# Kernel tuning notes

Hardware: AMD Instinct MI355X
Metric: run time of the kernel (lower is better)

Reference implementation:

```python
import jax, jax.numpy as jnp
from jax import lax
import numpy as np

BS, L, D, K, R, VOCAB = 4096, 200, 64, 4, 3, 100000
DROP = jnp.float32(-(1 << 31))


def squash(caps):
    # caps: (bs, K, D)
    n = jnp.linalg.norm(caps, axis=2, keepdims=True)   # (bs, K, 1)
    n2 = n * n
    return n2 / ((1.0 + n2) * n + 1e-9) * caps


def setup_inputs() -> dict:
    key = jax.random.key(0)
    ks = jax.random.split(key, 8)
    his = jax.random.randint(ks[0], (BS, L), 0, VOCAB)                     # item ids, 0 = pad
    E = jax.random.normal(ks[1], (VOCAB, D), dtype=jnp.float32)            # itemEmbeds.weight
    S = jax.random.normal(ks[2], (D, D), dtype=jnp.float32)                # bilinear map S
    B0 = jax.random.normal(ks[3], (K, L), dtype=jnp.float32)               # routing logits
    lim1 = 1.0 / np.sqrt(D)
    W1 = jax.random.uniform(ks[4], (D, 4 * D), jnp.float32, -lim1, lim1)   # dense1 (in, out)
    b1 = jax.random.uniform(ks[5], (4 * D,), jnp.float32, -lim1, lim1)
    lim2 = 1.0 / np.sqrt(4 * D)
    W2 = jax.random.uniform(ks[6], (4 * D, D), jnp.float32, -lim2, lim2)   # dense2 (in, out)
    b2 = jax.random.uniform(ks[7], (D,), jnp.float32, -lim2, lim2)
    return {"his": his, "E": E, "S": S, "B0": B0, "W1": W1, "b1": b1, "W2": W2, "b2": b2}


def reference(his, E, S, B0, W1, b1, W2, b2):
    bs = his.shape[0]
    # padding_idx=0 -> embedding row 0 is zero
    E = E.at[0].set(0.0)
    mask = (his != 0)[:, None, :]                       # (bs, 1, L), broadcasts over K
    hisP = jnp.einsum('bld,de->ble', E[his], S)         # (bs, L, D)
    hisPd = lax.stop_gradient(hisP)                     # routing updates run under no_grad
    B = jnp.broadcast_to(lax.stop_gradient(B0)[None], (bs, K, L))
    for _ in range(R - 1):
        W = jax.nn.softmax(jnp.where(mask, B, DROP), axis=2)   # (bs, K, L)
        caps = squash(jnp.einsum('bkl,bld->bkd', W, hisPd))
        B = B + jnp.einsum('bkd,bld->bkl', caps, hisPd)
    W = jax.nn.softmax(jnp.where(mask, B, DROP), axis=2)
    caps = squash(jnp.einsum('bkl,bld->bkd', W, hisP))         # differentiable last iter
    h = jax.nn.relu(jnp.einsum('bkd,df->bkf', caps, W1) + b1)
    return jnp.einsum('bkf,fd->bkd', h, W2) + b2               # (bs, K, D)
```

## Files before the change

### kernel.cpp

```cpp
#include <hip/hip_runtime.h>

#define LSEQ 200
#define KCAP 4
#define NVOC 100000

__device__ __forceinline__ void fma4(float4& a, float s, const float4& v) {
    a.x = fmaf(s, v.x, a.x); a.y = fmaf(s, v.y, a.y);
    a.z = fmaf(s, v.z, a.z); a.w = fmaf(s, v.w, a.w);
}

__global__ __launch_bounds__(256) void precompute_P(
    const float* __restrict__ E, const float* __restrict__ S,
    float* __restrict__ P)
{
    __shared__ __align__(16) float4 Sl4[1024];
    const int tid = threadIdx.x;
    #pragma unroll
    for (int t = tid; t < 1024; t += 256) Sl4[t] = ((const float4*)S)[t];
    __syncthreads();

    const int v = blockIdx.x * 256 + tid;
    const bool ok = (v < NVOC);
    const float4* __restrict__ Er = (const float4*)E + (size_t)(ok ? v : 0) * 16;

    float4 acc[16];
    #pragma unroll
    for (int j = 0; j < 16; j++) acc[j] = make_float4(0.f, 0.f, 0.f, 0.f);

    #pragma unroll 1
    for (int ec = 0; ec < 16; ec += 2) {
        float4 ea = Er[ec], eb = Er[ec + 1];
        float ev[8] = {ea.x, ea.y, ea.z, ea.w, eb.x, eb.y, eb.z, eb.w};
        #pragma unroll
        for (int e = 0; e < 8; e++) {
            const float4* Srow = Sl4 + (ec * 4 + e) * 16;
            #pragma unroll
            for (int j = 0; j < 16; j++) fma4(acc[j], ev[e], Srow[j]);
        }
    }
    if (ok) {
        float4* Pr = (float4*)P + (size_t)v * 16;
        if (v == 0) {
            #pragma unroll
            for (int j = 0; j < 16; j++) acc[j] = make_float4(0.f, 0.f, 0.f, 0.f);
        }
        #pragma unroll
        for (int j = 0; j < 16; j++) Pr[j] = acc[j];
    }
}

__global__ __launch_bounds__(256, 2) void mind_row(
    const int*   __restrict__ his, const float* __restrict__ P,
    const float* __restrict__ B0,  const float* __restrict__ W1,
    const float* __restrict__ b1,  const float* __restrict__ W2,
    const float* __restrict__ b2,  float* __restrict__ out)
{
    __shared__ __align__(16) float4 hisP4[LSEQ * 17];
    __shared__ __align__(16) float  W4[LSEQ * 4];
    __shared__ __align__(16) float  Bm[KCAP * LSEQ];
    __shared__ __align__(16) float  caps4[64 * 4];
    __shared__ __align__(16) float4 capsT4[KCAP * 16];
    __shared__ __align__(16) float4 part4[16 * 17];
    __shared__ float bigneg[LSEQ];
    __shared__ int   idxs[LSEQ];

    const int b = blockIdx.x, tid = threadIdx.x;
    const int lane = tid & 63, wv = tid >> 6;
    const int q = lane >> 4, r = lane & 15;

    for (int l = tid; l < LSEQ; l += 256) {
        int id = his[b * LSEQ + l];
        idxs[l]   = id;
        bigneg[l] = (id != 0) ? 0.f : -1e30f;
    }
    for (int t = tid; t < KCAP * LSEQ; t += 256) Bm[t] = B0[t];
    __syncthreads();

    float4 hp4[13];
    const float4* P4 = (const float4*)P;
    #pragma unroll
    for (int i = 0; i < 13; i++) {
        int  l     = wv * 50 + i * 4 + q;
        bool valid = (i < 12) || (q < 2);
        int  lc    = valid ? l : 0;
        float4 vv  = P4[(size_t)idxs[lc] * 16 + r];
        if (!valid) vv = make_float4(0.f, 0.f, 0.f, 0.f);
        hp4[i] = vv;
        if (valid) hisP4[l * 17 + r] = vv;
    }
    __syncthreads();

    for (int rr = 0; rr < 3; rr++) {
        {
            const float* Bk = Bm + wv * LSEQ;
            float x0 = Bk[lane]       + bigneg[lane];
            float x1 = Bk[lane + 64]  + bigneg[lane + 64];
            float x2 = Bk[lane + 128] + bigneg[lane + 128];
            float x3 = (lane < 8) ? (Bk[lane + 192] + bigneg[lane + 192]) : -3.0e38f;
            float m = fmaxf(fmaxf(x0, x1), fmaxf(x2, x3));
            #pragma unroll
            for (int off = 32; off; off >>= 1) m = fmaxf(m, __shfl_xor(m, off, 64));
            float e0 = __expf(x0 - m), e1 = __expf(x1 - m), e2 = __expf(x2 - m);
            float e3 = (lane < 8) ? __expf(x3 - m) : 0.f;
            float s = e0 + e1 + e2 + e3;
            #pragma unroll
            for (int off = 32; off; off >>= 1) s += __shfl_xor(s, off, 64);
            float inv = 1.f / s;
            W4[lane * 4 + wv]         = e0 * inv;
            W4[(lane + 64) * 4 + wv]  = e1 * inv;
            W4[(lane + 128) * 4 + wv] = e2 * inv;
            if (lane < 8) W4[(lane + 192) * 4 + wv] = e3 * inv;
        }
        __syncthreads();

        {
            float4 a0 = make_float4(0,0,0,0), a1 = a0, a2 = a0, a3 = a0;
            #pragma unroll
            for (int i = 0; i < 13; i++) {
                int l  = wv * 50 + i * 4 + q;
                int lc = (l < LSEQ - 1) ? l : (LSEQ - 1);
                float4 w = *(const float4*)(W4 + lc * 4);
                fma4(a0, w.x, hp4[i]); fma4(a1, w.y, hp4[i]);
                fma4(a2, w.z, hp4[i]); fma4(a3, w.w, hp4[i]);
            }
            #pragma unroll
            for (int off = 16; off <= 32; off <<= 1) {
                a0.x += __shfl_xor(a0.x, off, 64); a0.y += __shfl_xor(a0.y, off, 64);
                a0.z += __shfl_xor(a0.z, off, 64); a0.w += __shfl_xor(a0.w, off, 64);
                a1.x += __shfl_xor(a1.x, off, 64); a1.y += __shfl_xor(a1.y, off, 64);
                a1.z += __shfl_xor(a1.z, off, 64); a1.w += __shfl_xor(a1.w, off, 64);
                a2.x += __shfl_xor(a2.x, off, 64); a2.y += __shfl_xor(a2.y, off, 64);
                a2.z += __shfl_xor(a2.z, off, 64); a2.w += __shfl_xor(a2.w, off, 64);
                a3.x += __shfl_xor(a3.x, off, 64); a3.y += __shfl_xor(a3.y, off, 64);
                a3.z += __shfl_xor(a3.z, off, 64); a3.w += __shfl_xor(a3.w, off, 64);
            }
            if (q == 0) {
                part4[(wv * 4 + 0) * 17 + r] = a0;
                part4[(wv * 4 + 1) * 17 + r] = a1;
                part4[(wv * 4 + 2) * 17 + r] = a2;
                part4[(wv * 4 + 3) * 17 + r] = a3;
            }
        }
        __syncthreads();

        {
            const float* pf = (const float*)part4;
            float c = pf[(0 * 4 + wv) * 68 + lane] + pf[(1 * 4 + wv) * 68 + lane]
                    + pf[(2 * 4 + wv) * 68 + lane] + pf[(3 * 4 + wv) * 68 + lane];
            float n2 = c * c;
            #pragma unroll
            for (int off = 32; off; off >>= 1) n2 += __shfl_xor(n2, off, 64);
            float n  = sqrtf(n2);
            float sc = n2 / ((1.f + n2) * n + 1e-9f);
            c *= sc;
            caps4[lane * 4 + wv]          = c;
            ((float*)capsT4)[wv * 64 + lane] = c;
        }
        __syncthreads();

        if (rr < 2) {
            if (tid < LSEQ) {
                const int l = tid;
                float s0 = 0, s1 = 0, s2 = 0, s3 = 0;
                #pragma unroll
                for (int j = 0; j < 16; j++) {
                    float4 h  = hisP4[l * 17 + j];
                    float4 c0 = capsT4[j],      c1 = capsT4[16 + j];
                    float4 c2 = capsT4[32 + j], c3 = capsT4[48 + j];
                    s0 = fmaf(h.x, c0.x, fmaf(h.y, c0.y, fmaf(h.z, c0.z, fmaf(h.w, c0.w, s0))));
                    s1 = fmaf(h.x, c1.x, fmaf(h.y, c1.y, fmaf(h.z, c1.z, fmaf(h.w, c1.w, s1))));
                    s2 = fmaf(h.x, c2.x, fmaf(h.y, c2.y, fmaf(h.z, c2.z, fmaf(h.w, c2.w, s2))));
                    s3 = fmaf(h.x, c3.x, fmaf(h.y, c3.y, fmaf(h.z, c3.z, fmaf(h.w, c3.w, s3))));
                }
                Bm[l]       += s0;
                Bm[200 + l] += s1;
                Bm[400 + l] += s2;
                Bm[600 + l] += s3;
            }
            __syncthreads();
        }
    }

    float4* h44 = (float4*)hisP4;
    {
        const int f = tid;
        float h0 = 0, h1 = 0, h2 = 0, h3 = 0;
        #pragma unroll 8
        for (int d = 0; d < 64; d++) {
            float  w = W1[d * 256 + f];
            float4 c = *(const float4*)(caps4 + d * 4);
            h0 = fmaf(c.x, w, h0); h1 = fmaf(c.y, w, h1);
            h2 = fmaf(c.z, w, h2); h3 = fmaf(c.w, w, h3);
        }
        float bb = b1[f];
        h44[f] = make_float4(fmaxf(h0 + bb, 0.f), fmaxf(h1 + bb, 0.f),
                             fmaxf(h2 + bb, 0.f), fmaxf(h3 + bb, 0.f));
    }
    __syncthreads();
    float* partf = (float*)part4;
    {
        float o0 = 0, o1 = 0, o2 = 0, o3 = 0;
        #pragma unroll 8
        for (int i = 0; i < 64; i++) {
            int f = wv * 64 + i;
            float  w  = W2[f * 64 + lane];
            float4 hv = h44[f];
            o0 = fmaf(hv.x, w, o0); o1 = fmaf(hv.y, w, o1);
            o2 = fmaf(hv.z, w, o2); o3 = fmaf(hv.w, w, o3);
        }
        partf[wv * 256 + lane]       = o0;
        partf[wv * 256 + 64 + lane]  = o1;
        partf[wv * 256 + 128 + lane] = o2;
        partf[wv * 256 + 192 + lane] = o3;
    }
    __syncthreads();
    {
        float o = partf[wv * 64 + lane]       + partf[256 + wv * 64 + lane]
                + partf[512 + wv * 64 + lane] + partf[768 + wv * 64 + lane];
        out[b * 256 + tid] = o + b2[lane];
    }
}

extern "C" void kernel_launch(void* const* d_in, const int* in_sizes, int n_in,
                              void* d_out, int out_size, void* d_ws, size_t ws_size,
                              hipStream_t stream) {
    const int*   his = (const int*)  d_in[0];
    const float* E   = (const float*)d_in[1];
    const float* S   = (const float*)d_in[2];
    const float* B0  = (const float*)d_in[3];
    const float* W1  = (const float*)d_in[4];
    const float* b1  = (const float*)d_in[5];
    const float* W2  = (const float*)d_in[6];
    const float* b2  = (const float*)d_in[7];
    float* out = (float*)d_out;
    float* P   = (float*)d_ws;

    precompute_P<<<(NVOC + 255) / 256, 256, 0, stream>>>(E, S, P);
    mind_row<<<4096, 256, 0, stream>>>(his, P, B0, W1, b1, W2, b2, out);
}
```

Baseline: 256.3 us.

## Drop hisP LDS copy, reuse register-held rows with shuffles; split P precompute across waves

The routing-logit update now takes history rows from the registers loaded during the gather and reduces the dot products with xor shuffles, so the large padded hisP shared-memory buffer and one barrier are gone. With less LDS per block, launch bounds rise to 4 blocks per CU to increase occupancy. The embedding projection kernel now gives each wave 16 of the 64 output columns, reading S straight from global/cache instead of LDS. This lowers registers per thread in that kernel. The cost is more shuffle traffic and four times as many E row reads in the precompute.

```diff
diff --git a/kernel.cpp b/kernel.cpp
--- a/kernel.cpp
+++ b/kernel.cpp
@@ -13,54 +13,56 @@
     const float* __restrict__ E, const float* __restrict__ S,
     float* __restrict__ P)
 {
-    __shared__ __align__(16) float4 Sl4[1024];
-    const int tid = threadIdx.x;
+    const int tid  = threadIdx.x;
+    const int lane = tid & 63;
+    const int wvu  = __builtin_amdgcn_readfirstlane(tid >> 6);
+    const int row  = blockIdx.x * 64 + lane;
+    const bool ok  = (row < NVOC);
+
+    const float4* __restrict__ Er = (const float4*)E + (size_t)(ok ? row : 0) * 16;
+    const float4* __restrict__ S4 = (const float4*)S + wvu * 4;
+
+    float4 acc[4];
     #pragma unroll
-    for (int t = tid; t < 1024; t += 256) Sl4[t] = ((const float4*)S)[t];
-    __syncthreads();
-
-    const int v = blockIdx.x * 256 + tid;
-    const bool ok = (v < NVOC);
-    const float4* __restrict__ Er = (const float4*)E + (size_t)(ok ? v : 0) * 16;
-
-    float4 acc[16];
-    #pragma unroll
-    for (int j = 0; j < 16; j++) acc[j] = make_float4(0.f, 0.f, 0.f, 0.f);
-
-    #pragma unroll 1
-    for (int ec = 0; ec < 16; ec += 2) {
-        float4 ea = Er[ec], eb = Er[ec + 1];
-        float ev[8] = {ea.x, ea.y, ea.z, ea.w, eb.x, eb.y, eb.z, eb.w};
+    for (int j = 0; j < 4; j++) acc[j] = make_float4(0.f, 0.f, 0.f, 0.f);
+
+    #pragma unroll 4
+    for (int ec = 0; ec < 16; ec++) {
+        float4 ev = Er[ec];
+        float e4[4] = {ev.x, ev.y, ev.z, ev.w};
         #pragma unroll
-        for (int e = 0; e < 8; e++) {
-            const float4* Srow = Sl4 + (ec * 4 + e) * 16;
-            #pragma unroll
-            for (int j = 0; j < 16; j++) fma4(acc[j], ev[e], Srow[j]);
+        for (int u = 0; u < 4; u++) {
+            const int e = ec * 4 + u;
+            float4 s0 = S4[e * 16 + 0];
+            float4 s1 = S4[e * 16 + 1];
+            float4 s2 = S4[e * 16 + 2];
+            float4 s3 = S4[e * 16 + 3];
+            fma4(acc[0], e4[u], s0); fma4(acc[1], e4[u], s1);
+            fma4(acc[2], e4[u], s2); fma4(acc[3], e4[u], s3);
         }
     }
     if (ok) {
-        float4* Pr = (float4*)P + (size_t)v * 16;
-        if (v == 0) {
-            #pragma unroll
-            for (int j = 0; j < 16; j++) acc[j] = make_float4(0.f, 0.f, 0.f, 0.f);
-        }
-        #pragma unroll
-        for (int j = 0; j < 16; j++) Pr[j] = acc[j];
-    }
-}
-
-__global__ __launch_bounds__(256, 2) void mind_row(
+        if (row == 0) {
+            #pragma unroll
+            for (int j = 0; j < 4; j++) acc[j] = make_float4(0.f, 0.f, 0.f, 0.f);
+        }
+        float4* Pr = (float4*)P + (size_t)row * 16 + wvu * 4;
+        Pr[0] = acc[0]; Pr[1] = acc[1]; Pr[2] = acc[2]; Pr[3] = acc[3];
+    }
+}
+
+__global__ __launch_bounds__(256, 4) void mind_row(
     const int*   __restrict__ his, const float* __restrict__ P,
     const float* __restrict__ B0,  const float* __restrict__ W1,
     const float* __restrict__ b1,  const float* __restrict__ W2,
     const float* __restrict__ b2,  float* __restrict__ out)
 {
-    __shared__ __align__(16) float4 hisP4[LSEQ * 17];
     __shared__ __align__(16) float  W4[LSEQ * 4];
     __shared__ __align__(16) float  Bm[KCAP * LSEQ];
     __shared__ __align__(16) float  caps4[64 * 4];
     __shared__ __align__(16) float4 capsT4[KCAP * 16];
     __shared__ __align__(16) float4 part4[16 * 17];
+    __shared__ __align__(16) float4 h44[256];
     __shared__ float bigneg[LSEQ];
     __shared__ int   idxs[LSEQ];
 
@@ -86,9 +88,7 @@
         float4 vv  = P4[(size_t)idxs[lc] * 16 + r];
         if (!valid) vv = make_float4(0.f, 0.f, 0.f, 0.f);
         hp4[i] = vv;
-        if (valid) hisP4[l * 17 + r] = vv;
-    }
-    __syncthreads();
+    }
 
     for (int rr = 0; rr < 3; rr++) {
         {
@@ -153,35 +153,40 @@
             float n  = sqrtf(n2);
             float sc = n2 / ((1.f + n2) * n + 1e-9f);
             c *= sc;
-            caps4[lane * 4 + wv]          = c;
+            caps4[lane * 4 + wv]             = c;
             ((float*)capsT4)[wv * 64 + lane] = c;
         }
         __syncthreads();
 
         if (rr < 2) {
-            if (tid < LSEQ) {
-                const int l = tid;
-                float s0 = 0, s1 = 0, s2 = 0, s3 = 0;
+            float4 c0 = capsT4[0 * 16 + r];
+            float4 c1 = capsT4[1 * 16 + r];
+            float4 c2 = capsT4[2 * 16 + r];
+            float4 c3 = capsT4[3 * 16 + r];
+            #pragma unroll
+            for (int i = 0; i < 13; i++) {
+                float4 v = hp4[i];
+                float p0 = fmaf(v.x, c0.x, fmaf(v.y, c0.y, fmaf(v.z, c0.z, v.w * c0.w)));
+                float p1 = fmaf(v.x, c1.x, fmaf(v.y, c1.y, fmaf(v.z, c1.z, v.w * c1.w)));
+                float p2 = fmaf(v.x, c2.x, fmaf(v.y, c2.y, fmaf(v.z, c2.z, v.w * c2.w)));
+                float p3 = fmaf(v.x, c3.x, fmaf(v.y, c3.y, fmaf(v.z, c3.z, v.w * c3.w)));
                 #pragma unroll
-                for (int j = 0; j < 16; j++) {
-                    float4 h  = hisP4[l * 17 + j];
-                    float4 c0 = capsT4[j],      c1 = capsT4[16 + j];
-                    float4 c2 = capsT4[32 + j], c3 = capsT4[48 + j];
-                    s0 = fmaf(h.x, c0.x, fmaf(h.y, c0.y, fmaf(h.z, c0.z, fmaf(h.w, c0.w, s0))));
-                    s1 = fmaf(h.x, c1.x, fmaf(h.y, c1.y, fmaf(h.z, c1.z, fmaf(h.w, c1.w, s1))));
-                    s2 = fmaf(h.x, c2.x, fmaf(h.y, c2.y, fmaf(h.z, c2.z, fmaf(h.w, c2.w, s2))));
-                    s3 = fmaf(h.x, c3.x, fmaf(h.y, c3.y, fmaf(h.z, c3.z, fmaf(h.w, c3.w, s3))));
+                for (int off = 1; off < 16; off <<= 1) {
+                    p0 += __shfl_xor(p0, off, 64);
+                    p1 += __shfl_xor(p1, off, 64);
+                    p2 += __shfl_xor(p2, off, 64);
+                    p3 += __shfl_xor(p3, off, 64);
                 }
-                Bm[l]       += s0;
-                Bm[200 + l] += s1;
-                Bm[400 + l] += s2;
-                Bm[600 + l] += s3;
+                if (r < 4 && ((i < 12) || (q < 2))) {
+                    int l = wv * 50 + i * 4 + q;
+                    float p = (r == 0) ? p0 : (r == 1) ? p1 : (r == 2) ? p2 : p3;
+                    Bm[r * 200 + l] += p;
+                }
             }
             __syncthreads();
         }
     }
 
-    float4* h44 = (float4*)hisP4;
     {
         const int f = tid;
         float h0 = 0, h1 = 0, h2 = 0, h3 = 0;
@@ -235,6 +240,6 @@
     float* out = (float*)d_out;
     float* P   = (float*)d_ws;
 
-    precompute_P<<<(NVOC + 255) / 256, 256, 0, stream>>>(E, S, P);
+    precompute_P<<<(NVOC + 63) / 64, 256, 0, stream>>>(E, S, P);
     mind_row<<<4096, 256, 0, stream>>>(his, P, B0, W1, b1, W2, b2, out);
 }
```

After: 262.2 us. +2.3%, slower.

## Fuse projection into routing kernel by applying S to capsules, not embeddings

Applied to the files above, without the earlier changes.

Drops the precompute pass that multiplied all 100k vocabulary embeddings by S. The single fused kernel gathers raw embedding rows and moves S onto the capsule side: it forms W·E, then multiplies by S, and for the routing update it uses E·(S·caps). Routing logits and masks also move from shared memory into registers. This removes a 25.6 MB write and read of the projected table plus the vocab-wide GEMM, at the cost of small per-row 64x64 matvecs against S read from global memory in every routing iteration.

```diff
diff --git a/kernel.cpp b/kernel.cpp
--- a/kernel.cpp
+++ b/kernel.cpp
@@ -2,110 +2,72 @@
 
 #define LSEQ 200
 #define KCAP 4
-#define NVOC 100000
 
 __device__ __forceinline__ void fma4(float4& a, float s, const float4& v) {
     a.x = fmaf(s, v.x, a.x); a.y = fmaf(s, v.y, a.y);
     a.z = fmaf(s, v.z, a.z); a.w = fmaf(s, v.w, a.w);
 }
 
-__global__ __launch_bounds__(256) void precompute_P(
-    const float* __restrict__ E, const float* __restrict__ S,
-    float* __restrict__ P)
+__global__ __launch_bounds__(256, 2) void mind_fused(
+    const int*   __restrict__ his, const float* __restrict__ E,
+    const float* __restrict__ S,   const float* __restrict__ B0,
+    const float* __restrict__ W1,  const float* __restrict__ b1,
+    const float* __restrict__ W2,  const float* __restrict__ b2,
+    float* __restrict__ out)
 {
-    __shared__ __align__(16) float4 Sl4[1024];
-    const int tid = threadIdx.x;
-    #pragma unroll
-    for (int t = tid; t < 1024; t += 256) Sl4[t] = ((const float4*)S)[t];
-    __syncthreads();
-
-    const int v = blockIdx.x * 256 + tid;
-    const bool ok = (v < NVOC);
-    const float4* __restrict__ Er = (const float4*)E + (size_t)(ok ? v : 0) * 16;
-
-    float4 acc[16];
-    #pragma unroll
-    for (int j = 0; j < 16; j++) acc[j] = make_float4(0.f, 0.f, 0.f, 0.f);
-
-    #pragma unroll 1
-    for (int ec = 0; ec < 16; ec += 2) {
-        float4 ea = Er[ec], eb = Er[ec + 1];
-        float ev[8] = {ea.x, ea.y, ea.z, ea.w, eb.x, eb.y, eb.z, eb.w};
-        #pragma unroll
-        for (int e = 0; e < 8; e++) {
-            const float4* Srow = Sl4 + (ec * 4 + e) * 16;
-            #pragma unroll
-            for (int j = 0; j < 16; j++) fma4(acc[j], ev[e], Srow[j]);
-        }
-    }
-    if (ok) {
-        float4* Pr = (float4*)P + (size_t)v * 16;
-        if (v == 0) {
-            #pragma unroll
-            for (int j = 0; j < 16; j++) acc[j] = make_float4(0.f, 0.f, 0.f, 0.f);
-        }
-        #pragma unroll
-        for (int j = 0; j < 16; j++) Pr[j] = acc[j];
-    }
-}
-
-__global__ __launch_bounds__(256, 2) void mind_row(
-    const int*   __restrict__ his, const float* __restrict__ P,
-    const float* __restrict__ B0,  const float* __restrict__ W1,
-    const float* __restrict__ b1,  const float* __restrict__ W2,
-    const float* __restrict__ b2,  float* __restrict__ out)
-{
-    __shared__ __align__(16) float4 hisP4[LSEQ * 17];
+    __shared__ __align__(16) float4 Er4[LSEQ * 17];
     __shared__ __align__(16) float  W4[LSEQ * 4];
-    __shared__ __align__(16) float  Bm[KCAP * LSEQ];
+    __shared__ __align__(16) float4 part4[16 * 16];
+    __shared__ __align__(16) float  cbuf[256];
+    __shared__ __align__(16) float  capsL[256];
     __shared__ __align__(16) float  caps4[64 * 4];
-    __shared__ __align__(16) float4 capsT4[KCAP * 16];
-    __shared__ __align__(16) float4 part4[16 * 17];
-    __shared__ float bigneg[LSEQ];
-    __shared__ int   idxs[LSEQ];
+
+    int* idxs = (int*)cbuf;
 
     const int b = blockIdx.x, tid = threadIdx.x;
     const int lane = tid & 63, wv = tid >> 6;
     const int q = lane >> 4, r = lane & 15;
 
-    for (int l = tid; l < LSEQ; l += 256) {
-        int id = his[b * LSEQ + l];
-        idxs[l]   = id;
-        bigneg[l] = (id != 0) ? 0.f : -1e30f;
-    }
-    for (int t = tid; t < KCAP * LSEQ; t += 256) Bm[t] = B0[t];
-    __syncthreads();
+    for (int l = tid; l < LSEQ; l += 256) idxs[l] = his[b * LSEQ + l];
+    __syncthreads();
+
+    float Breg[4], msk[4];
+    #pragma unroll
+    for (int s = 0; s < 4; s++) {
+        int l = lane + 64 * s;
+        bool in = (l < LSEQ);
+        Breg[s] = in ? B0[wv * LSEQ + l] : 0.f;
+        msk[s]  = (in && idxs[l] != 0) ? 0.f : -3.0e38f;
+    }
 
     float4 hp4[13];
-    const float4* P4 = (const float4*)P;
+    const float4* E4 = (const float4*)E;
     #pragma unroll
     for (int i = 0; i < 13; i++) {
         int  l     = wv * 50 + i * 4 + q;
         bool valid = (i < 12) || (q < 2);
-        int  lc    = valid ? l : 0;
-        float4 vv  = P4[(size_t)idxs[lc] * 16 + r];
-        if (!valid) vv = make_float4(0.f, 0.f, 0.f, 0.f);
+        int  lc    = valid ? l : (wv * 50);
+        int  id    = idxs[lc];
+        float4 vv  = E4[(size_t)id * 16 + r];
+        if (id == 0 || !valid) vv = make_float4(0.f, 0.f, 0.f, 0.f);
         hp4[i] = vv;
-        if (valid) hisP4[l * 17 + r] = vv;
+        if (valid) Er4[l * 17 + r] = vv;
     }
     __syncthreads();
 
     for (int rr = 0; rr < 3; rr++) {
         {
-            const float* Bk = Bm + wv * LSEQ;
-            float x0 = Bk[lane]       + bigneg[lane];
-            float x1 = Bk[lane + 64]  + bigneg[lane + 64];
-            float x2 = Bk[lane + 128] + bigneg[lane + 128];
-            float x3 = (lane < 8) ? (Bk[lane + 192] + bigneg[lane + 192]) : -3.0e38f;
+            float x0 = Breg[0] + msk[0], x1 = Breg[1] + msk[1];
+            float x2 = Breg[2] + msk[2], x3 = Breg[3] + msk[3];
             float m = fmaxf(fmaxf(x0, x1), fmaxf(x2, x3));
             #pragma unroll
             for (int off = 32; off; off >>= 1) m = fmaxf(m, __shfl_xor(m, off, 64));
-            float e0 = __expf(x0 - m), e1 = __expf(x1 - m), e2 = __expf(x2 - m);
-            float e3 = (lane < 8) ? __expf(x3 - m) : 0.f;
-            float s = e0 + e1 + e2 + e3;
-            #pragma unroll
-            for (int off = 32; off; off >>= 1) s += __shfl_xor(s, off, 64);
-            float inv = 1.f / s;
+            float e0 = __expf(x0 - m), e1 = __expf(x1 - m);
+            float e2 = __expf(x2 - m), e3 = __expf(x3 - m);
+            float ssum = e0 + e1 + e2 + e3;
+            #pragma unroll
+            for (int off = 32; off; off >>= 1) ssum += __shfl_xor(ssum, off, 64);
+            float inv = 1.f / ssum;
             W4[lane * 4 + wv]         = e0 * inv;
             W4[(lane + 64) * 4 + wv]  = e1 * inv;
             W4[(lane + 128) * 4 + wv] = e2 * inv;
@@ -135,53 +97,77 @@
                 a3.z += __shfl_xor(a3.z, off, 64); a3.w += __shfl_xor(a3.w, off, 64);
             }
             if (q == 0) {
-                part4[(wv * 4 + 0) * 17 + r] = a0;
-                part4[(wv * 4 + 1) * 17 + r] = a1;
-                part4[(wv * 4 + 2) * 17 + r] = a2;
-                part4[(wv * 4 + 3) * 17 + r] = a3;
+                part4[(wv * 4 + 0) * 16 + r] = a0;
+                part4[(wv * 4 + 1) * 16 + r] = a1;
+                part4[(wv * 4 + 2) * 16 + r] = a2;
+                part4[(wv * 4 + 3) * 16 + r] = a3;
             }
         }
         __syncthreads();
 
         {
             const float* pf = (const float*)part4;
-            float c = pf[(0 * 4 + wv) * 68 + lane] + pf[(1 * 4 + wv) * 68 + lane]
-                    + pf[(2 * 4 + wv) * 68 + lane] + pf[(3 * 4 + wv) * 68 + lane];
-            float n2 = c * c;
+            float ce = pf[(0 * 4 + wv) * 64 + lane] + pf[(1 * 4 + wv) * 64 + lane]
+                     + pf[(2 * 4 + wv) * 64 + lane] + pf[(3 * 4 + wv) * 64 + lane];
+            cbuf[wv * 64 + lane] = ce;
+        }
+        __syncthreads();
+
+        {
+            float cd = 0.f;
+            #pragma unroll 4
+            for (int e = 0; e < 64; e += 4) {
+                float4 cc = *(const float4*)(cbuf + wv * 64 + e);
+                cd = fmaf(cc.x, S[(e + 0) * 64 + lane], cd);
+                cd = fmaf(cc.y, S[(e + 1) * 64 + lane], cd);
+                cd = fmaf(cc.z, S[(e + 2) * 64 + lane], cd);
+                cd = fmaf(cc.w, S[(e + 3) * 64 + lane], cd);
+            }
+            float n2 = cd * cd;
             #pragma unroll
             for (int off = 32; off; off >>= 1) n2 += __shfl_xor(n2, off, 64);
             float n  = sqrtf(n2);
             float sc = n2 / ((1.f + n2) * n + 1e-9f);
-            c *= sc;
-            caps4[lane * 4 + wv]          = c;
-            ((float*)capsT4)[wv * 64 + lane] = c;
+            float c  = cd * sc;
+            caps4[lane * 4 + wv] = c;
+            capsL[wv * 64 + lane] = c;
         }
         __syncthreads();
 
         if (rr < 2) {
-            if (tid < LSEQ) {
-                const int l = tid;
-                float s0 = 0, s1 = 0, s2 = 0, s3 = 0;
+            {
+                const float4* S4 = (const float4*)S;
+                float cs = 0.f;
                 #pragma unroll
                 for (int j = 0; j < 16; j++) {
-                    float4 h  = hisP4[l * 17 + j];
-                    float4 c0 = capsT4[j],      c1 = capsT4[16 + j];
-                    float4 c2 = capsT4[32 + j], c3 = capsT4[48 + j];
-                    s0 = fmaf(h.x, c0.x, fmaf(h.y, c0.y, fmaf(h.z, c0.z, fmaf(h.w, c0.w, s0))));
-                    s1 = fmaf(h.x, c1.x, fmaf(h.y, c1.y, fmaf(h.z, c1.z, fmaf(h.w, c1.w, s1))));
-                    s2 = fmaf(h.x, c2.x, fmaf(h.y, c2.y, fmaf(h.z, c2.z, fmaf(h.w, c2.w, s2))));
-                    s3 = fmaf(h.x, c3.x, fmaf(h.y, c3.y, fmaf(h.z, c3.z, fmaf(h.w, c3.w, s3))));
+                    float4 sv = S4[(size_t)lane * 16 + j];
+                    float4 cv = *(const float4*)(capsL + wv * 64 + j * 4);
+                    cs = fmaf(sv.x, cv.x, fmaf(sv.y, cv.y,
+                         fmaf(sv.z, cv.z, fmaf(sv.w, cv.w, cs))));
                 }
-                Bm[l]       += s0;
-                Bm[200 + l] += s1;
-                Bm[400 + l] += s2;
-                Bm[600 + l] += s3;
+                cbuf[wv * 64 + lane] = cs;
             }
             __syncthreads();
-        }
-    }
-
-    float4* h44 = (float4*)hisP4;
+
+            #pragma unroll
+            for (int s = 0; s < 4; s++) {
+                int l = lane + 64 * s;
+                if (l < LSEQ) {
+                    float dsum = 0.f;
+                    #pragma unroll
+                    for (int j = 0; j < 16; j++) {
+                        float4 ev = Er4[l * 17 + j];
+                        float4 cv = *(const float4*)(cbuf + wv * 64 + j * 4);
+                        dsum = fmaf(ev.x, cv.x, fmaf(ev.y, cv.y,
+                               fmaf(ev.z, cv.z, fmaf(ev.w, cv.w, dsum))));
+                    }
+                    Breg[s] += dsum;
+                }
+            }
+        }
+    }
+
+    float4* h44 = (float4*)Er4;
     {
         const int f = tid;
         float h0 = 0, h1 = 0, h2 = 0, h3 = 0;
@@ -233,8 +219,7 @@
     const float* W2  = (const float*)d_in[6];
     const float* b2  = (const float*)d_in[7];
     float* out = (float*)d_out;
-    float* P   = (float*)d_ws;
-
-    precompute_P<<<(NVOC + 255) / 256, 256, 0, stream>>>(E, S, P);
-    mind_row<<<4096, 256, 0, stream>>>(his, P, B0, W1, b1, W2, b2, out);
+    (void)d_ws; (void)ws_size;
+
+    mind_fused<<<4096, 256, 0, stream>>>(his, E, S, B0, W1, b1, W2, b2, out);
 }
```

Measured after the change: 276.3 us. +7.8%, slower.
